# Kernel tuning notes

Hardware: AMD Instinct MI355X
Metric: run time of the kernel (lower is better)

Reference implementation:

```python
import jax, jax.numpy as jnp
import numpy as np

EPS = 1e-6  # GLOBAL_EPS
D_QK = 192
ATTN_DIM = 768


def setup_inputs() -> dict:
    key = jax.random.key(0)
    ks = jax.random.split(key, 12)
    B, C, H, W = 16, 192, 56, 56
    d_qk, d_v = D_QK, 2 * D_QK
    attn_dim, inner = ATTN_DIM, d_v
    r = lambda k, s, sc=0.05: jax.random.normal(k, s, dtype=jnp.float32) * sc
    return {
        "x": jax.random.normal(ks[0], (B, C, H, W), dtype=jnp.float32),
        "proj_w": r(ks[1], (attn_dim, C)),          # 1x1 conv + BN folded
        "proj_b": r(ks[2], (attn_dim,)),
        "dwc_w": r(ks[3], (attn_dim, 1, 3, 3)),     # depthwise 3x3, BN folded
        "dwc_b": r(ks[4], (attn_dim,)),
        "g_w": r(ks[5], (inner, attn_dim)),          # ConvGate pointwise conv1d
        "g_b": r(ks[6], (inner,)),
        "an_w": 1.0 + r(ks[7], (inner,)),            # RMSNorm weight
        "sv": 1.0 + r(ks[8], (inner,)),              # Scale(inner, (1, inner, 1))
        "out_w": r(ks[9], (C, inner)),               # 1x1 conv + BN folded
        "out_b": r(ks[10], (C,)),
    }


def reference(x, proj_w, proj_b, dwc_w, dwc_b, g_w, g_b, an_w, sv, out_w, out_b):
    B, C, H, W = x.shape
    d_qk = D_QK
    # proj: ConvNorm 1x1 (conv + BN folded to affine)
    y = jnp.einsum("bchw,oc->bohw", x, proj_w) + proj_b[None, :, None, None]
    # dwc: RepConv depthwise 3x3 with residual (res=True)
    dw = jax.lax.conv_general_dilated(
        y, dwc_w, window_strides=(1, 1), padding="SAME",
        dimension_numbers=("NCHW", "OIHW", "NCHW"),
        feature_group_count=ATTN_DIM)
    y = dw + dwc_b[None, :, None, None] + y
    # flatten spatial -> tokens, split q/k/v along channels
    xs = y.reshape(B, ATTN_DIM, H * W)            # (B, attn_dim, N)
    q, k, v = xs[:, :d_qk], xs[:, d_qk:2 * d_qk], xs[:, 2 * d_qk:]
    # linear_attn: feature map = silu, scale = N**-0.5
    qf = jax.nn.silu(q)                            # (B, d_qk, N)
    kf = jax.nn.silu(k)
    N = H * W
    s = N ** -0.5
    # use_linear branch (N >> d): z = kT.mean(-2,True) @ q + eps ; attn = (v s)(kT s) q
    z = jnp.einsum("bd,bdn->bn", kf.mean(-1), qf)[:, None, :] + EPS  # (B, 1, N)
    vk = jnp.einsum("bvn,bdn->bvd", v * s, kf * s)  # (B, d_v, d_qk)
    attn = jnp.einsum("bvd,bdn->bvn", vk, qf) / z   # (B, d_v, N)
    # gate: pointwise conv1d on full projected features + sigmoid
    gate = jax.nn.sigmoid(jnp.einsum("bcn,oc->bon", xs, g_w) + g_b[None, :, None])
    attn = attn * gate
    # attn_norm (RMS over channels) + scale_v(v) residual
    rms = jnp.sqrt(jnp.mean(attn * attn, axis=1, keepdims=True) + EPS)
    attn = attn / rms * an_w[None, :, None] + v * sv[None, :, None]
    # out: ConvNorm 1x1 back to dim
    o = attn.reshape(B, -1, H, W)
    return jnp.einsum("bchw,oc->bohw", o, out_w) + out_b[None, :, None, None]
```

## Files before the change

kernel.cpp:

```cpp
#include <hip/hip_runtime.h>
#include <hip/hip_bf16.h>

typedef unsigned short u16;
typedef __attribute__((ext_vector_type(8))) short bf16x8;
typedef __attribute__((ext_vector_type(4))) float f32x4;

constexpr int B_ = 16, C_ = 192, H_ = 56, W_ = 56;
constexpr int N_ = H_ * W_;
constexpr int A_ = 768;
constexpr int Dq = 192;
constexpr int Vd = 384;
constexpr float EPSf = 1e-6f;

union U8 { bf16x8 v; u16 s[8]; unsigned u[4]; };

__device__ __forceinline__ float bits2f(u16 u) {
  return __uint_as_float(((unsigned)u) << 16);
}
__device__ __forceinline__ u16 f2bits(float f) {
  __hip_bfloat16 h = __float2bfloat16(f);
  u16 u;
  __builtin_memcpy(&u, &h, sizeof(u));
  return u;
}
__device__ __forceinline__ float silu_f(float v) { return v / (1.0f + __expf(-v)); }
__device__ __forceinline__ float sigm_f(float v) { return 1.0f / (1.0f + __expf(-v)); }

__device__ __forceinline__ f32x4 MFMA(bf16x8 a, bf16x8 b, f32x4 c) {
  return __builtin_amdgcn_mfma_f32_16x16x32_bf16(a, b, c, 0, 0, 0);
}

__global__ __launch_bounds__(256) void k_prep(const float* __restrict__ pw,
                                              const float* __restrict__ gw,
                                              const float* __restrict__ ow,
                                              u16* __restrict__ pwb,
                                              u16* __restrict__ gwb,
                                              u16* __restrict__ owb) {
  const int bid = blockIdx.x;
  const size_t base = ((size_t)bid * 256 + threadIdx.x) * 8;
  const float* src;
  u16* dst;
  size_t off;
  if (bid < 72) { src = pw; dst = pwb; off = base; }
  else if (bid < 216) { src = gw; dst = gwb; off = base - 147456; }
  else { src = ow; dst = owb; off = base - 442368; }
  float4 v0 = *(const float4*)&src[off];
  float4 v1 = *(const float4*)&src[off + 4];
  U8 r;
  r.s[0] = f2bits(v0.x); r.s[1] = f2bits(v0.y); r.s[2] = f2bits(v0.z); r.s[3] = f2bits(v0.w);
  r.s[4] = f2bits(v1.x); r.s[5] = f2bits(v1.y); r.s[6] = f2bits(v1.z); r.s[7] = f2bits(v1.w);
  *(bf16x8*)&dst[off] = r.v;
}

__global__ __launch_bounds__(256) void k_proj(const float* __restrict__ x,
                                              const u16* __restrict__ pwb,
                                              const float* __restrict__ pb,
                                              u16* __restrict__ y0t) {
  const int n0 = blockIdx.x * 64;
  const int oy = blockIdx.y;
  const int b = blockIdx.z;
  __shared__ u16 Xt[64][200];
  __shared__ u16 Wa[256][32];
  const int t = threadIdx.x;
  const int lane = t & 63, wid = t >> 6;
  const int fr = lane & 15, fg = lane >> 4;

  {
    const int p = t & 31, co = t >> 5;
    const float* xb = x + (size_t)b * C_ * N_ + n0 + 2 * p;
#pragma unroll
    for (int rnd = 0; rnd < 3; ++rnd) {
      const int c0 = rnd * 64 + co * 8;
      float2 v[8];
#pragma unroll
      for (int i = 0; i < 8; ++i) v[i] = *(const float2*)&xb[(size_t)(c0 + i) * N_];
      U8 r0, r1;
#pragma unroll
      for (int i = 0; i < 8; ++i) { r0.s[i] = f2bits(v[i].x); r1.s[i] = f2bits(v[i].y); }
      *(bf16x8*)&Xt[2 * p][c0] = r0.v;
      *(bf16x8*)&Xt[2 * p + 1][c0] = r1.v;
    }
  }

  f32x4 acc[4][4];
#pragma unroll
  for (int mi = 0; mi < 4; ++mi)
#pragma unroll
    for (int ni = 0; ni < 4; ++ni) acc[mi][ni] = (f32x4){0.f, 0.f, 0.f, 0.f};

  const int orow_c = t >> 2, oct_c = t & 3;
  for (int ks = 0; ks < 6; ++ks) {
    __syncthreads();
#pragma unroll
    for (int jj = 0; jj < 4; ++jj) {
      const int orow = orow_c + 64 * jj;
      const int sw = (orow >> 1) & 3;
      bf16x8 v = *(const bf16x8*)&pwb[(size_t)(oy * 256 + orow) * C_ + ks * 32 + oct_c * 8];
      *(bf16x8*)&Wa[orow][(oct_c ^ sw) * 8] = v;
    }
    __syncthreads();
    bf16x8 bfrag[4];
#pragma unroll
    for (int ni = 0; ni < 4; ++ni)
      bfrag[ni] = *(const bf16x8*)&Xt[ni * 16 + fr][ks * 32 + fg * 8];
#pragma unroll
    for (int mi = 0; mi < 4; ++mi) {
      const int ar = wid * 64 + mi * 16 + fr;
      bf16x8 a = *(const bf16x8*)&Wa[ar][(fg ^ ((ar >> 1) & 3)) * 8];
#pragma unroll
      for (int ni = 0; ni < 4; ++ni) acc[mi][ni] = MFMA(a, bfrag[ni], acc[mi][ni]);
    }
  }
#pragma unroll
  for (int mi = 0; mi < 4; ++mi) {
    const int o4 = oy * 256 + wid * 64 + mi * 16 + fg * 4;
    const float b0 = pb[o4], b1 = pb[o4 + 1], b2 = pb[o4 + 2], b3 = pb[o4 + 3];
#pragma unroll
    for (int ni = 0; ni < 4; ++ni) {
      const int n = n0 + ni * 16 + fr;
      ushort4 pk;
      pk.x = f2bits(acc[mi][ni][0] + b0);
      pk.y = f2bits(acc[mi][ni][1] + b1);
      pk.z = f2bits(acc[mi][ni][2] + b2);
      pk.w = f2bits(acc[mi][ni][3] + b3);
      *(ushort4*)&y0t[((size_t)b * N_ + n) * A_ + o4] = pk;
    }
  }
}

__global__ __launch_bounds__(256) void k_dwc(const u16* __restrict__ y0t,
                                             const float* __restrict__ cw,
                                             const float* __restrict__ cb,
                                             u16* __restrict__ yt,
                                             u16* __restrict__ skq) {
  const int pid = blockIdx.x;
  const int L = (pid & 7) * 336 + (pid >> 3);
  const int h = L % 56, at = (L / 56) % 3, b = L / 168;
  const int t = threadIdx.x;
  const int a = at * 256 + (t & 31) * 8;
  const int wl = t >> 5;
  float w9[9][8];
  float bias[8];
#pragma unroll
  for (int j = 0; j < 8; ++j) {
    bias[j] = cb[a + j];
#pragma unroll
    for (int k = 0; k < 9; ++k) w9[k][j] = cw[(a + j) * 9 + k];
  }
  const u16* src = y0t + (size_t)b * N_ * A_ + a;
  u16* dst = yt + (size_t)b * N_ * A_ + a;
  const bool hok0 = h > 0, hok2 = h < 55;
  for (int wc = 0; wc < 7; ++wc) {
    const int w = wc * 8 + wl;
    const bool wok0 = w > 0, wok2 = w < 55;
    U8 nb[9];
#pragma unroll
    for (int dh = -1; dh <= 1; ++dh) {
      const bool hok = (dh == -1) ? hok0 : ((dh == 1) ? hok2 : true);
#pragma unroll
      for (int dw = -1; dw <= 1; ++dw) {
        const int k = (dh + 1) * 3 + (dw + 1);
        const bool ok = hok && ((dw == -1) ? wok0 : ((dw == 1) ? wok2 : true));
        if (ok)
          nb[k].v = *(const bf16x8*)&src[(size_t)((h + dh) * 56 + (w + dw)) * A_];
        else
          nb[k].u[0] = nb[k].u[1] = nb[k].u[2] = nb[k].u[3] = 0u;
      }
    }
    U8 o;
    float sv[8];
#pragma unroll
    for (int j = 0; j < 8; ++j) {
      float s = bias[j] + bits2f(nb[4].s[j]);
#pragma unroll
      for (int k = 0; k < 9; ++k) s = fmaf(w9[k][j], bits2f(nb[k].s[j]), s);
      sv[j] = s;
      o.s[j] = f2bits(s);
    }
    *(bf16x8*)&dst[(size_t)(h * 56 + w) * A_] = o.v;
    if (a < 384) {
      U8 q;
#pragma unroll
      for (int j = 0; j < 8; ++j) q.s[j] = f2bits(silu_f(sv[j]));
      *(bf16x8*)&skq[((size_t)b * N_ + h * 56 + w) * 384 + a] = q.v;
    }
  }
}

__global__ __launch_bounds__(256) void k_kfmean(const u16* __restrict__ skq,
                                                float* __restrict__ kfp) {
  const int ns = blockIdx.x, dc = blockIdx.y, b = blockIdx.z;
  const int t = threadIdx.x;
  const int dq = t & 15, nw = t >> 4;
  const u16* p = skq + ((size_t)b * N_ + ns * 448 + nw) * 384 + 192 + dc * 64 + dq * 4;
  float s0 = 0, s1 = 0, s2 = 0, s3 = 0;
#pragma unroll 4
  for (int i = 0; i < 28; ++i) {
    ushort4 u = *(const ushort4*)&p[(size_t)i * 16 * 384];
    s0 += bits2f(u.x);
    s1 += bits2f(u.y);
    s2 += bits2f(u.z);
    s3 += bits2f(u.w);
  }
  __shared__ float red[16][65];
  red[nw][dq * 4 + 0] = s0;
  red[nw][dq * 4 + 1] = s1;
  red[nw][dq * 4 + 2] = s2;
  red[nw][dq * 4 + 3] = s3;
  __syncthreads();
  if (t < 64) {
    float s = 0;
#pragma unroll
    for (int i = 0; i < 16; ++i) s += red[i][t];
    kfp[((size_t)ns * B_ + b) * Dq + dc * 64 + t] = s * (1.0f / (float)N_);
  }
}

__global__ __launch_bounds__(256) void k_z(const u16* __restrict__ skq,
                                           const float* __restrict__ kfp,
                                           float* __restrict__ zinv) {
  const int b = blockIdx.y;
  const int n = blockIdx.x * 256 + threadIdx.x;
  __shared__ float kf[192];
  if (threadIdx.x < 192) {
    float s = 0;
#pragma unroll
    for (int ns = 0; ns < 7; ++ns) s += kfp[((size_t)ns * B_ + b) * Dq + threadIdx.x];
    kf[threadIdx.x] = s;
  }
  __syncthreads();
  if (n < N_) {
    const u16* p = skq + ((size_t)b * N_ + n) * 384;
    float z = 0;
#pragma unroll
    for (int j = 0; j < 24; ++j) {
      U8 u;
      u.v = *(const bf16x8*)&p[j * 8];
#pragma unroll
      for (int i = 0; i < 8; ++i) z = fmaf(kf[j * 8 + i], bits2f(u.s[i]), z);
    }
    zinv[(size_t)b * N_ + n] = 1.0f / (z + EPSf);
  }
}

__global__ __launch_bounds__(256) void k_vk(const u16* __restrict__ skq,
                                            const u16* __restrict__ yt,
                                            float* __restrict__ vkpart) {
  const int pid = blockIdx.x;
  const int L = (pid & 7) * 42 + (pid >> 3);
  const int ns = L % 7;
  const int vblk = (L / 7) % 3;
  const int b = L / 21;
  const int t = threadIdx.x;
  const int lane = t & 63, wid = t >> 6;
  const int fr = lane & 15, fg = lane >> 4;
  const int vbase = (wid >> 1) * 64, dbase = (wid & 1) * 96;

  __shared__ u16 T[320 * 64];
  unsigned* T32 = (unsigned*)T;

  const int oct0 = t & 7;
  const int pair = (t >> 3) & 31;
  const int nb0 = ns * 448;

  U8 pre[5][2];
  auto load_pre = [&](int n0) {
    const int n = nb0 + n0 + pair * 2;
#pragma unroll
    for (int j = 0; j < 5; ++j) {
      const int oct = oct0 + 8 * j;
      const u16* srcp;
      size_t stride;
      if (j < 3) {
        srcp = skq + ((size_t)b * N_ + n) * 384 + 192 + oct * 8;
        stride = 384;
      } else {
        srcp = yt + ((size_t)b * N_ + n) * A_ + 384 + vblk * 128 + (oct - 24) * 8;
        stride = A_;
      }
      pre[j][0].v = *(const bf16x8*)srcp;
      pre[j][1].v = *(const bf16x8*)(srcp + stride);
    }
  };

  f32x4 acc[4][6];
#pragma unroll
  for (int mi = 0; mi < 4; ++mi)
#pragma unroll
    for (int ni = 0; ni < 6; ++ni) acc[mi][ni] = (f32x4){0.f, 0.f, 0.f, 0.f};

  load_pre(0);
  for (int s = 0; s < 7; ++s) {
    __syncthreads();
#pragma unroll
    for (int j = 0; j < 5; ++j) {
      const int rowb = (oct0 + 8 * j) * 8;
#pragma unroll
      for (int i = 0; i < 8; ++i) {
        const int row = rowb + i;
        const int sw = (row & 7) ^ ((row >> 3) & 7);
        const unsigned val =
            ((unsigned)pre[j][0].s[i] & 0xffffu) | (((unsigned)pre[j][1].s[i]) << 16);
        T32[row * 32 + (pair ^ (sw << 2))] = val;
      }
    }
    __syncthreads();
    if (s < 6) load_pre((s + 1) * 64);
#pragma unroll
    for (int kf2 = 0; kf2 < 2; ++kf2) {
      bf16x8 bfrag[6];
#pragma unroll
      for (int ni = 0; ni < 6; ++ni) {
        const int row = dbase + ni * 16 + fr;
        const int sw = (row & 7) ^ ((row >> 3) & 7);
        bfrag[ni] = *(const bf16x8*)&T[row * 64 + ((kf2 * 32 + fg * 8) ^ (sw << 3))];
      }
#pragma unroll
      for (int mi = 0; mi < 4; ++mi) {
        const int row = 192 + vbase + mi * 16 + fr;
        const int sw = (row & 7) ^ ((row >> 3) & 7);
        bf16x8 a = *(const bf16x8*)&T[row * 64 + ((kf2 * 32 + fg * 8) ^ (sw << 3))];
#pragma unroll
        for (int ni = 0; ni < 6; ++ni) acc[mi][ni] = MFMA(a, bfrag[ni], acc[mi][ni]);
      }
    }
  }
  float* base = vkpart + (((size_t)ns * 16 + b) * 3 + vblk) * (128 * 192);
#pragma unroll
  for (int mi = 0; mi < 4; ++mi)
#pragma unroll
    for (int ni = 0; ni < 6; ++ni) {
      const int v = vbase + mi * 16 + fg * 4;
      const int d = dbase + ni * 16 + fr;
      float* o = base + (size_t)v * 192 + d;
      o[0] = acc[mi][ni][0];
      o[192] = acc[mi][ni][1];
      o[384] = acc[mi][ni][2];
      o[576] = acc[mi][ni][3];
    }
}

__global__ __launch_bounds__(256) void k_vkred(const float* __restrict__ vkpart,
                                               u16* __restrict__ vkb) {
  const size_t e = ((size_t)blockIdx.x * 256 + threadIdx.x) * 8;
  constexpr size_t NSSTRIDE = (size_t)16 * 3 * 128 * 192;
  float4 s0 = {0, 0, 0, 0}, s1 = {0, 0, 0, 0};
#pragma unroll
  for (int ns = 0; ns < 7; ++ns) {
    float4 a0 = *(const float4*)&vkpart[ns * NSSTRIDE + e];
    float4 a1 = *(const float4*)&vkpart[ns * NSSTRIDE + e + 4];
    s0.x += a0.x; s0.y += a0.y; s0.z += a0.z; s0.w += a0.w;
    s1.x += a1.x; s1.y += a1.y; s1.z += a1.z; s1.w += a1.w;
  }
  const float sc = 1.0f / (float)N_;
  U8 r;
  r.s[0] = f2bits(s0.x * sc); r.s[1] = f2bits(s0.y * sc);
  r.s[2] = f2bits(s0.z * sc); r.s[3] = f2bits(s0.w * sc);
  r.s[4] = f2bits(s1.x * sc); r.s[5] = f2bits(s1.y * sc);
  r.s[6] = f2bits(s1.z * sc); r.s[7] = f2bits(s1.w * sc);
  *(bf16x8*)&vkb[e] = r.v;
}

__global__ __launch_bounds__(256, 3) void k_gateattn(const u16* __restrict__ yt,
                                                     const u16* __restrict__ skq,
                                                     const float* __restrict__ zinv,
                                                     const u16* __restrict__ vkb,
                                                     const u16* __restrict__ gwb,
                                                     const float* __restrict__ gb,
                                                     u16* __restrict__ attnt) {
  const int pid = blockIdx.x;
  const int L = (pid & 7) * 196 + (pid >> 3);
  const int vh = L & 1;
  const int n0 = ((L >> 1) % 49) * 64;
  const int b = L / 98;
  const int t = threadIdx.x;
  const int lane = t & 63, wid = t >> 6, wm = wid >> 1, wn = wid & 1;
  const int fr = lane & 15, fg = lane >> 4;
  __shared__ u16 Wa[192][40];
  __shared__ u16 Xt[64][40];
  __shared__ float zl[64];
  if (t < 64) zl[t] = zinv[(size_t)b * N_ + n0 + t];
  const u16* yb = yt + ((size_t)b * N_ + n0) * A_;
  const u16* qb = skq + ((size_t)b * N_ + n0) * 384;

  f32x4 acc[6][2];
#pragma unroll
  for (int mi = 0; mi < 6; ++mi)
#pragma unroll
    for (int ni = 0; ni < 2; ++ni) acc[mi][ni] = (f32x4){0.f, 0.f, 0.f, 0.f};

  for (int ks = 0; ks < 6; ++ks) {
    {
      const int o = t >> 2, cs = t & 3;
#pragma unroll
      for (int rr = 0; rr < 3; ++rr) {
        const int v = rr * 64 + o;
        *(bf16x8*)&Wa[v][cs * 8] =
            *(const bf16x8*)&vkb[((size_t)(vh * 192 + v) + 0) * 0 +
                                 ((size_t)b * Vd + vh * 192 + v) * 192 + ks * 32 + cs * 8];
      }
    }
    {
      const int n = t >> 2, aq = t & 3;
      *(bf16x8*)&Xt[n][aq * 8] = *(const bf16x8*)&qb[(size_t)n * 384 + ks * 32 + aq * 8];
    }
    __syncthreads();
    bf16x8 bfr[2];
#pragma unroll
    for (int ni = 0; ni < 2; ++ni) bfr[ni] = *(const bf16x8*)&Xt[wn * 32 + ni * 16 + fr][fg * 8];
#pragma unroll
    for (int mi = 0; mi < 6; ++mi) {
      bf16x8 a = *(const bf16x8*)&Wa[wm * 96 + mi * 16 + fr][fg * 8];
      acc[mi][0] = MFMA(a, bfr[0], acc[mi][0]);
      acc[mi][1] = MFMA(a, bfr[1], acc[mi][1]);
    }
    __syncthreads();
  }

  uint2 pp[6][2];
#pragma unroll
  for (int mi = 0; mi < 6; ++mi)
#pragma unroll
    for (int ni = 0; ni < 2; ++ni) {
      const float z = zl[wn * 32 + ni * 16 + fr];
      unsigned a0 = ((unsigned)f2bits(acc[mi][ni][0] * z) & 0xffffu) |
                    (((unsigned)f2bits(acc[mi][ni][1] * z) & 0xffffu) << 16);
      unsigned a1 = ((unsigned)f2bits(acc[mi][ni][2] * z) & 0xffffu) |
                    (((unsigned)f2bits(acc[mi][ni][3] * z) & 0xffffu) << 16);
      pp[mi][ni] = make_uint2(a0, a1);
      acc[mi][ni] = (f32x4){0.f, 0.f, 0.f, 0.f};
    }

  for (int ks = 0; ks < 24; ++ks) {
    {
      const int o = t >> 2, cs = t & 3;
#pragma unroll
      for (int rr = 0; rr < 3; ++rr) {
        const int v = rr * 64 + o;
        *(bf16x8*)&Wa[v][cs * 8] =
            *(const bf16x8*)&gwb[(size_t)(vh * 192 + v) * A_ + ks * 32 + cs * 8];
      }
    }
    {
      const int n = t >> 2, aq = t & 3;
      *(bf16x8*)&Xt[n][aq * 8] = *(const bf16x8*)&yb[(size_t)n * A_ + ks * 32 + aq * 8];
    }
    __syncthreads();
    bf16x8 bfr[2];
#pragma unroll
    for (int ni = 0; ni < 2; ++ni) bfr[ni] = *(const bf16x8*)&Xt[wn * 32 + ni * 16 + fr][fg * 8];
#pragma unroll
    for (int mi = 0; mi < 6; ++mi) {
      bf16x8 a = *(const bf16x8*)&Wa[wm * 96 + mi * 16 + fr][fg * 8];
      acc[mi][0] = MFMA(a, bfr[0], acc[mi][0]);
      acc[mi][1] = MFMA(a, bfr[1], acc[mi][1]);
    }
    __syncthreads();
  }

#pragma unroll
  for (int mi = 0; mi < 6; ++mi) {
    const int vb = vh * 192 + wm * 96 + mi * 16 + fg * 4;
    const float g0 = gb[vb], g1 = gb[vb + 1], g2 = gb[vb + 2], g3 = gb[vb + 3];
#pragma unroll
    for (int ni = 0; ni < 2; ++ni) {
      const int n = n0 + wn * 32 + ni * 16 + fr;
      const uint2 p = pp[mi][ni];
      const float pv0 = bits2f((u16)(p.x & 0xffffu)), pv1 = bits2f((u16)(p.x >> 16));
      const float pv2 = bits2f((u16)(p.y & 0xffffu)), pv3 = bits2f((u16)(p.y >> 16));
      ushort4 o;
      o.x = f2bits(pv0 * sigm_f(acc[mi][ni][0] + g0));
      o.y = f2bits(pv1 * sigm_f(acc[mi][ni][1] + g1));
      o.z = f2bits(pv2 * sigm_f(acc[mi][ni][2] + g2));
      o.w = f2bits(pv3 * sigm_f(acc[mi][ni][3] + g3));
      *(ushort4*)&attnt[((size_t)b * N_ + n) * Vd + vb] = o;
    }
  }
}

__global__ __launch_bounds__(256) void k_rmsfinal(const u16* __restrict__ yt,
                                                  const float* __restrict__ anw,
                                                  const float* __restrict__ svw,
                                                  u16* __restrict__ attnt) {
  const int b = blockIdx.y;
  const int n0 = blockIdx.x * 32;
  const int t = threadIdx.x;
  __shared__ float anws[384], svws[384];
  for (int i = t; i < 384; i += 256) {
    anws[i] = anw[i];
    svws[i] = svw[i];
  }
  __syncthreads();
  const int n = n0 + (t >> 3);
  const int vs = (t & 7) * 8;
  u16* ap = attnt + ((size_t)b * N_ + n) * Vd;
  U8 av[6];
  float ss = 0.f;
#pragma unroll
  for (int j = 0; j < 6; ++j) {
    av[j].v = *(const bf16x8*)&ap[vs + j * 64];
#pragma unroll
    for (int i = 0; i < 8; ++i) {
      const float f = bits2f(av[j].s[i]);
      ss = fmaf(f, f, ss);
    }
  }
  ss += __shfl_xor(ss, 1);
  ss += __shfl_xor(ss, 2);
  ss += __shfl_xor(ss, 4);
  const float rinv = rsqrtf(ss * (1.0f / (float)Vd) + EPSf);
  const u16* vp = yt + ((size_t)b * N_ + n) * A_ + 2 * Dq;
#pragma unroll
  for (int j = 0; j < 6; ++j) {
    U8 vv, o;
    vv.v = *(const bf16x8*)&vp[vs + j * 64];
#pragma unroll
    for (int i = 0; i < 8; ++i) {
      const int v = vs + j * 64 + i;
      const float val = bits2f(av[j].s[i]) * rinv * anws[v] + bits2f(vv.s[i]) * svws[v];
      o.s[i] = f2bits(val);
    }
    *(bf16x8*)&ap[vs + j * 64] = o.v;
  }
}

__global__ __launch_bounds__(256, 2) void k_out(const u16* __restrict__ attnt,
                                                const u16* __restrict__ owb,
                                                const float* __restrict__ ob,
                                                float* __restrict__ out) {
  const int n0 = blockIdx.x * 64;
  const int b = blockIdx.y;
  __shared__ u16 Xt[64][392];
  __shared__ u16 Wa[64][40];
  const int t = threadIdx.x;
  const int lane = t & 63, wid = t >> 6, wm = wid >> 1, wn = wid & 1;
  const int fr = lane & 15, fg = lane >> 4;
  {
    const int n = t >> 2, aq = t & 3;
    const u16* src = attnt + ((size_t)b * N_ + n0 + n) * Vd + aq * 8;
#pragma unroll
    for (int vr = 0; vr < 12; ++vr)
      *(bf16x8*)&Xt[n][vr * 32 + aq * 8] = *(const bf16x8*)&src[vr * 32];
  }
  f32x4 acc[2][2];
  for (int cb = 0; cb < 3; ++cb) {
#pragma unroll
    for (int mi = 0; mi < 2; ++mi)
#pragma unroll
      for (int ni = 0; ni < 2; ++ni) acc[mi][ni] = (f32x4){0.f, 0.f, 0.f, 0.f};
    for (int ks = 0; ks < 12; ++ks) {
      {
        const int o = t >> 2, cs = t & 3;
        *(bf16x8*)&Wa[o][cs * 8] =
            *(const bf16x8*)&owb[(size_t)(cb * 64 + o) * Vd + ks * 32 + cs * 8];
      }
      __syncthreads();
      bf16x8 a0 = *(const bf16x8*)&Wa[wm * 32 + fr][fg * 8];
      bf16x8 a1 = *(const bf16x8*)&Wa[wm * 32 + 16 + fr][fg * 8];
      bf16x8 b0 = *(const bf16x8*)&Xt[wn * 32 + fr][ks * 32 + fg * 8];
      bf16x8 b1 = *(const bf16x8*)&Xt[wn * 32 + 16 + fr][ks * 32 + fg * 8];
      acc[0][0] = MFMA(a0, b0, acc[0][0]);
      acc[0][1] = MFMA(a0, b1, acc[0][1]);
      acc[1][0] = MFMA(a1, b0, acc[1][0]);
      acc[1][1] = MFMA(a1, b1, acc[1][1]);
      __syncthreads();
    }
#pragma unroll
    for (int mi = 0; mi < 2; ++mi) {
      const int c = cb * 64 + wm * 32 + mi * 16 + fg * 4;
      const float b0 = ob[c], b1 = ob[c + 1], b2 = ob[c + 2], b3 = ob[c + 3];
#pragma unroll
      for (int ni = 0; ni < 2; ++ni) {
        const int n = n0 + wn * 32 + ni * 16 + fr;
        float* o = out + ((size_t)b * C_ + c) * N_ + n;
        o[0 * N_] = acc[mi][ni][0] + b0;
        o[1 * N_] = acc[mi][ni][1] + b1;
        o[2 * N_] = acc[mi][ni][2] + b2;
        o[3 * N_] = acc[mi][ni][3] + b3;
      }
    }
  }
}

extern "C" void kernel_launch(void* const* d_in, const int* in_sizes, int n_in,
                              void* d_out, int out_size, void* d_ws, size_t ws_size,
                              hipStream_t stream) {
  (void)in_sizes; (void)n_in; (void)out_size; (void)ws_size;
  const float* x = (const float*)d_in[0];
  const float* pw = (const float*)d_in[1];
  const float* pb = (const float*)d_in[2];
  const float* cw = (const float*)d_in[3];
  const float* cb = (const float*)d_in[4];
  const float* gw = (const float*)d_in[5];
  const float* gb = (const float*)d_in[6];
  const float* anw = (const float*)d_in[7];
  const float* svw = (const float*)d_in[8];
  const float* ow = (const float*)d_in[9];
  const float* ob = (const float*)d_in[10];
  float* out = (float*)d_out;

  char* ws = (char*)d_ws;
  const size_t szY = (size_t)B_ * N_ * A_ * 2;
  u16* y0t = (u16*)(ws);
  u16* attnt = (u16*)(ws);
  float* vkpart = (float*)(ws + 38535168);
  u16* vkb = (u16*)(ws + 71565312);
  u16* yt = (u16*)(ws + szY);
  u16* skq = (u16*)(ws + 2 * szY);
  char* ws2 = ws + 2 * szY + 38535168;
  float* kfp = (float*)(ws2);
  float* zinv = (float*)(ws2 + 86016);
  u16* pwb = (u16*)(ws2 + 86016 + 200704);
  u16* gwb = (u16*)(ws2 + 86016 + 200704 + 294912);
  u16* owb = (u16*)(ws2 + 86016 + 200704 + 294912 + 589824);

  k_prep<<<dim3(252), 256, 0, stream>>>(pw, gw, ow, pwb, gwb, owb);
  k_proj<<<dim3(49, 3, 16), 256, 0, stream>>>(x, pwb, pb, y0t);
  k_dwc<<<dim3(2688), 256, 0, stream>>>(y0t, cw, cb, yt, skq);
  k_kfmean<<<dim3(7, 3, 16), 256, 0, stream>>>(skq, kfp);
  k_z<<<dim3(13, 16), 256, 0, stream>>>(skq, kfp, zinv);
  k_vk<<<dim3(336), 256, 0, stream>>>(skq, yt, vkpart);
  k_vkred<<<dim3(576), 256, 0, stream>>>(vkpart, vkb);
  k_gateattn<<<dim3(1568), 256, 0, stream>>>(yt, skq, zinv, vkb, gwb, gb, attnt);
  k_rmsfinal<<<dim3(98, 16), 256, 0, stream>>>(yt, anw, svw, attnt);
  k_out<<<dim3(49, 16), 256, 0, stream>>>(attnt, owb, ob, out);
}
```

Measured before the change: 316.1 us.

## Register-prefetch global tiles and widen K steps in GEMM kernels

Measured after the change: 272.6 us. 1.16x faster.

```diff
diff --git a/kernel.cpp b/kernel.cpp
--- a/kernel.cpp
+++ b/kernel.cpp
@@ -89,20 +89,31 @@
     for (int ni = 0; ni < 4; ++ni) acc[mi][ni] = (f32x4){0.f, 0.f, 0.f, 0.f};
 
   const int orow_c = t >> 2, oct_c = t & 3;
+  U8 wreg[4];
+#pragma unroll
+  for (int jj = 0; jj < 4; ++jj)
+    wreg[jj].v = *(const bf16x8*)&pwb[(size_t)(oy * 256 + orow_c + 64 * jj) * C_ + oct_c * 8];
+
   for (int ks = 0; ks < 6; ++ks) {
     __syncthreads();
 #pragma unroll
     for (int jj = 0; jj < 4; ++jj) {
       const int orow = orow_c + 64 * jj;
       const int sw = (orow >> 1) & 3;
-      bf16x8 v = *(const bf16x8*)&pwb[(size_t)(oy * 256 + orow) * C_ + ks * 32 + oct_c * 8];
-      *(bf16x8*)&Wa[orow][(oct_c ^ sw) * 8] = v;
-    }
-    __syncthreads();
+      *(bf16x8*)&Wa[orow][(oct_c ^ sw) * 8] = wreg[jj].v;
+    }
+    __syncthreads();
+    if (ks < 5) {
+#pragma unroll
+      for (int jj = 0; jj < 4; ++jj)
+        wreg[jj].v = *(const bf16x8*)&pwb[(size_t)(oy * 256 + orow_c + 64 * jj) * C_ +
+                                          (ks + 1) * 32 + oct_c * 8];
+    }
     bf16x8 bfrag[4];
 #pragma unroll
     for (int ni = 0; ni < 4; ++ni)
       bfrag[ni] = *(const bf16x8*)&Xt[ni * 16 + fr][ks * 32 + fg * 8];
+    __builtin_amdgcn_s_setprio(1);
 #pragma unroll
     for (int mi = 0; mi < 4; ++mi) {
       const int ar = wid * 64 + mi * 16 + fr;
@@ -110,6 +121,7 @@
 #pragma unroll
       for (int ni = 0; ni < 4; ++ni) acc[mi][ni] = MFMA(a, bfrag[ni], acc[mi][ni]);
     }
+    __builtin_amdgcn_s_setprio(0);
   }
 #pragma unroll
   for (int mi = 0; mi < 4; ++mi) {
@@ -306,6 +318,7 @@
     }
     __syncthreads();
     if (s < 6) load_pre((s + 1) * 64);
+    __builtin_amdgcn_s_setprio(1);
 #pragma unroll
     for (int kf2 = 0; kf2 < 2; ++kf2) {
       bf16x8 bfrag[6];
@@ -324,6 +337,7 @@
         for (int ni = 0; ni < 6; ++ni) acc[mi][ni] = MFMA(a, bfrag[ni], acc[mi][ni]);
       }
     }
+    __builtin_amdgcn_s_setprio(0);
   }
   float* base = vkpart + (((size_t)ns * 16 + b) * 3 + vblk) * (128 * 192);
 #pragma unroll
@@ -361,13 +375,13 @@
   *(bf16x8*)&vkb[e] = r.v;
 }
 
-__global__ __launch_bounds__(256, 3) void k_gateattn(const u16* __restrict__ yt,
-                                                     const u16* __restrict__ skq,
-                                                     const float* __restrict__ zinv,
-                                                     const u16* __restrict__ vkb,
-                                                     const u16* __restrict__ gwb,
-                                                     const float* __restrict__ gb,
-                                                     u16* __restrict__ attnt) {
+__global__ __launch_bounds__(256) void k_gateattn(const u16* __restrict__ yt,
+                                                  const u16* __restrict__ skq,
+                                                  const float* __restrict__ zinv,
+                                                  const u16* __restrict__ vkb,
+                                                  const u16* __restrict__ gwb,
+                                                  const float* __restrict__ gb,
+                                                  u16* __restrict__ attnt) {
   const int pid = blockIdx.x;
   const int L = (pid & 7) * 196 + (pid >> 3);
   const int vh = L & 1;
@@ -376,86 +390,92 @@
   const int t = threadIdx.x;
   const int lane = t & 63, wid = t >> 6, wm = wid >> 1, wn = wid & 1;
   const int fr = lane & 15, fg = lane >> 4;
-  __shared__ u16 Wa[192][40];
-  __shared__ u16 Xt[64][40];
+  __shared__ u16 Wa[192][104];
+  __shared__ u16 Xt[64][104];
   __shared__ float zl[64];
   if (t < 64) zl[t] = zinv[(size_t)b * N_ + n0 + t];
   const u16* yb = yt + ((size_t)b * N_ + n0) * A_;
   const u16* qb = skq + ((size_t)b * N_ + n0) * 384;
+  const u16* wb0 = vkb + ((size_t)b * Vd + vh * 192) * 192;
+  const u16* wb1 = gwb + (size_t)(vh * 192) * A_;
+
+  int wrow[9], woc[9];
+#pragma unroll
+  for (int j = 0; j < 9; ++j) { const int idx = j * 256 + t; wrow[j] = idx / 12; woc[j] = idx % 12; }
+  int xrow[3], xoc[3];
+#pragma unroll
+  for (int j = 0; j < 3; ++j) { const int idx = j * 256 + t; xrow[j] = idx / 12; xoc[j] = idx % 12; }
+
+  U8 wreg[9], xreg[3];
+  auto loadW = [&](int ph, int ks0) {
+#pragma unroll
+    for (int j = 0; j < 9; ++j) {
+      const u16* s = ph ? (wb1 + (size_t)wrow[j] * A_ + ks0 + woc[j] * 8)
+                        : (wb0 + (size_t)wrow[j] * 192 + ks0 + woc[j] * 8);
+      wreg[j].v = *(const bf16x8*)s;
+    }
+  };
+  auto loadX = [&](int ph, int ks0) {
+#pragma unroll
+    for (int j = 0; j < 3; ++j) {
+      const u16* s = ph ? (yb + (size_t)xrow[j] * A_ + ks0 + xoc[j] * 8)
+                        : (qb + (size_t)xrow[j] * 384 + ks0 + xoc[j] * 8);
+      xreg[j].v = *(const bf16x8*)s;
+    }
+  };
 
   f32x4 acc[6][2];
 #pragma unroll
   for (int mi = 0; mi < 6; ++mi)
 #pragma unroll
     for (int ni = 0; ni < 2; ++ni) acc[mi][ni] = (f32x4){0.f, 0.f, 0.f, 0.f};
-
-  for (int ks = 0; ks < 6; ++ks) {
-    {
-      const int o = t >> 2, cs = t & 3;
-#pragma unroll
-      for (int rr = 0; rr < 3; ++rr) {
-        const int v = rr * 64 + o;
-        *(bf16x8*)&Wa[v][cs * 8] =
-            *(const bf16x8*)&vkb[((size_t)(vh * 192 + v) + 0) * 0 +
-                                 ((size_t)b * Vd + vh * 192 + v) * 192 + ks * 32 + cs * 8];
+  uint2 pp[6][2];
+
+  loadW(0, 0);
+  loadX(0, 0);
+  for (int it = 0; it < 10; ++it) {
+    __syncthreads();
+#pragma unroll
+    for (int j = 0; j < 9; ++j) *(bf16x8*)&Wa[wrow[j]][woc[j] * 8] = wreg[j].v;
+#pragma unroll
+    for (int j = 0; j < 3; ++j) *(bf16x8*)&Xt[xrow[j]][xoc[j] * 8] = xreg[j].v;
+    __syncthreads();
+    if (it < 9) {
+      const int nit = it + 1;
+      const int ph = nit >= 2;
+      const int ks0 = ph ? (nit - 2) * 96 : nit * 96;
+      loadW(ph, ks0);
+      loadX(ph, ks0);
+    }
+    __builtin_amdgcn_s_setprio(1);
+#pragma unroll
+    for (int kf = 0; kf < 3; ++kf) {
+      bf16x8 bfr[2];
+#pragma unroll
+      for (int ni = 0; ni < 2; ++ni)
+        bfr[ni] = *(const bf16x8*)&Xt[wn * 32 + ni * 16 + fr][kf * 32 + fg * 8];
+#pragma unroll
+      for (int mi = 0; mi < 6; ++mi) {
+        bf16x8 a = *(const bf16x8*)&Wa[wm * 96 + mi * 16 + fr][kf * 32 + fg * 8];
+        acc[mi][0] = MFMA(a, bfr[0], acc[mi][0]);
+        acc[mi][1] = MFMA(a, bfr[1], acc[mi][1]);
       }
     }
-    {
-      const int n = t >> 2, aq = t & 3;
-      *(bf16x8*)&Xt[n][aq * 8] = *(const bf16x8*)&qb[(size_t)n * 384 + ks * 32 + aq * 8];
-    }
-    __syncthreads();
-    bf16x8 bfr[2];
-#pragma unroll
-    for (int ni = 0; ni < 2; ++ni) bfr[ni] = *(const bf16x8*)&Xt[wn * 32 + ni * 16 + fr][fg * 8];
-#pragma unroll
-    for (int mi = 0; mi < 6; ++mi) {
-      bf16x8 a = *(const bf16x8*)&Wa[wm * 96 + mi * 16 + fr][fg * 8];
-      acc[mi][0] = MFMA(a, bfr[0], acc[mi][0]);
-      acc[mi][1] = MFMA(a, bfr[1], acc[mi][1]);
-    }
-    __syncthreads();
-  }
-
-  uint2 pp[6][2];
-#pragma unroll
-  for (int mi = 0; mi < 6; ++mi)
-#pragma unroll
-    for (int ni = 0; ni < 2; ++ni) {
-      const float z = zl[wn * 32 + ni * 16 + fr];
-      unsigned a0 = ((unsigned)f2bits(acc[mi][ni][0] * z) & 0xffffu) |
-                    (((unsigned)f2bits(acc[mi][ni][1] * z) & 0xffffu) << 16);
-      unsigned a1 = ((unsigned)f2bits(acc[mi][ni][2] * z) & 0xffffu) |
-                    (((unsigned)f2bits(acc[mi][ni][3] * z) & 0xffffu) << 16);
-      pp[mi][ni] = make_uint2(a0, a1);
-      acc[mi][ni] = (f32x4){0.f, 0.f, 0.f, 0.f};
-    }
-
-  for (int ks = 0; ks < 24; ++ks) {
-    {
-      const int o = t >> 2, cs = t & 3;
-#pragma unroll
-      for (int rr = 0; rr < 3; ++rr) {
-        const int v = rr * 64 + o;
-        *(bf16x8*)&Wa[v][cs * 8] =
-            *(const bf16x8*)&gwb[(size_t)(vh * 192 + v) * A_ + ks * 32 + cs * 8];
-      }
-    }
-    {
-      const int n = t >> 2, aq = t & 3;
-      *(bf16x8*)&Xt[n][aq * 8] = *(const bf16x8*)&yb[(size_t)n * A_ + ks * 32 + aq * 8];
-    }
-    __syncthreads();
-    bf16x8 bfr[2];
-#pragma unroll
-    for (int ni = 0; ni < 2; ++ni) bfr[ni] = *(const bf16x8*)&Xt[wn * 32 + ni * 16 + fr][fg * 8];
-#pragma unroll
-    for (int mi = 0; mi < 6; ++mi) {
-      bf16x8 a = *(const bf16x8*)&Wa[wm * 96 + mi * 16 + fr][fg * 8];
-      acc[mi][0] = MFMA(a, bfr[0], acc[mi][0]);
-      acc[mi][1] = MFMA(a, bfr[1], acc[mi][1]);
-    }
-    __syncthreads();
+    __builtin_amdgcn_s_setprio(0);
+    if (it == 1) {
+#pragma unroll
+      for (int mi = 0; mi < 6; ++mi)
+#pragma unroll
+        for (int ni = 0; ni < 2; ++ni) {
+          const float z = zl[wn * 32 + ni * 16 + fr];
+          unsigned a0 = ((unsigned)f2bits(acc[mi][ni][0] * z) & 0xffffu) |
+                        (((unsigned)f2bits(acc[mi][ni][1] * z) & 0xffffu) << 16);
+          unsigned a1 = ((unsigned)f2bits(acc[mi][ni][2] * z) & 0xffffu) |
+                        (((unsigned)f2bits(acc[mi][ni][3] * z) & 0xffffu) << 16);
+          pp[mi][ni] = make_uint2(a0, a1);
+          acc[mi][ni] = (f32x4){0.f, 0.f, 0.f, 0.f};
+        }
+    }
   }
 
 #pragma unroll
@@ -524,60 +544,85 @@
   }
 }
 
-__global__ __launch_bounds__(256, 2) void k_out(const u16* __restrict__ attnt,
-                                                const u16* __restrict__ owb,
-                                                const float* __restrict__ ob,
-                                                float* __restrict__ out) {
+__global__ __launch_bounds__(256) void k_out(const u16* __restrict__ attnt,
+                                             const u16* __restrict__ owb,
+                                             const float* __restrict__ ob,
+                                             float* __restrict__ out) {
   const int n0 = blockIdx.x * 64;
   const int b = blockIdx.y;
-  __shared__ u16 Xt[64][392];
-  __shared__ u16 Wa[64][40];
+  __shared__ u16 Wa[192][104];
+  __shared__ u16 Xt[64][104];
   const int t = threadIdx.x;
   const int lane = t & 63, wid = t >> 6, wm = wid >> 1, wn = wid & 1;
   const int fr = lane & 15, fg = lane >> 4;
-  {
-    const int n = t >> 2, aq = t & 3;
-    const u16* src = attnt + ((size_t)b * N_ + n0 + n) * Vd + aq * 8;
-#pragma unroll
-    for (int vr = 0; vr < 12; ++vr)
-      *(bf16x8*)&Xt[n][vr * 32 + aq * 8] = *(const bf16x8*)&src[vr * 32];
-  }
-  f32x4 acc[2][2];
-  for (int cb = 0; cb < 3; ++cb) {
-#pragma unroll
-    for (int mi = 0; mi < 2; ++mi)
-#pragma unroll
-      for (int ni = 0; ni < 2; ++ni) acc[mi][ni] = (f32x4){0.f, 0.f, 0.f, 0.f};
-    for (int ks = 0; ks < 12; ++ks) {
-      {
-        const int o = t >> 2, cs = t & 3;
-        *(bf16x8*)&Wa[o][cs * 8] =
-            *(const bf16x8*)&owb[(size_t)(cb * 64 + o) * Vd + ks * 32 + cs * 8];
+  const u16* xb = attnt + ((size_t)b * N_ + n0) * Vd;
+
+  int wrow[9], woc[9];
+#pragma unroll
+  for (int j = 0; j < 9; ++j) { const int idx = j * 256 + t; wrow[j] = idx / 12; woc[j] = idx % 12; }
+  int xrow[3], xoc[3];
+#pragma unroll
+  for (int j = 0; j < 3; ++j) { const int idx = j * 256 + t; xrow[j] = idx / 12; xoc[j] = idx % 12; }
+
+  U8 wreg[9], xreg[3];
+  auto loadW = [&](int ks0) {
+#pragma unroll
+    for (int j = 0; j < 9; ++j)
+      wreg[j].v = *(const bf16x8*)&owb[(size_t)wrow[j] * Vd + ks0 + woc[j] * 8];
+  };
+  auto loadX = [&](int ks0) {
+#pragma unroll
+    for (int j = 0; j < 3; ++j)
+      xreg[j].v = *(const bf16x8*)&xb[(size_t)xrow[j] * Vd + ks0 + xoc[j] * 8];
+  };
+
+  f32x4 acc[6][2];
+#pragma unroll
+  for (int mi = 0; mi < 6; ++mi)
+#pragma unroll
+    for (int ni = 0; ni < 2; ++ni) acc[mi][ni] = (f32x4){0.f, 0.f, 0.f, 0.f};
+
+  loadW(0);
+  loadX(0);
+  for (int it = 0; it < 4; ++it) {
+    __syncthreads();
+#pragma unroll
+    for (int j = 0; j < 9; ++j) *(bf16x8*)&Wa[wrow[j]][woc[j] * 8] = wreg[j].v;
+#pragma unroll
+    for (int j = 0; j < 3; ++j) *(bf16x8*)&Xt[xrow[j]][xoc[j] * 8] = xreg[j].v;
+    __syncthreads();
+    if (it < 3) {
+      loadW((it + 1) * 96);
+      loadX((it + 1) * 96);
+    }
+    __builtin_amdgcn_s_setprio(1);
+#pragma unroll
+    for (int kf = 0; kf < 3; ++kf) {
+      bf16x8 bfr[2];
+#pragma unroll
+      for (int ni = 0; ni < 2; ++ni)
+        bfr[ni] = *(const bf16x8*)&Xt[wn * 32 + ni * 16 + fr][kf * 32 + fg * 8];
+#pragma unroll
+      for (int mi = 0; mi < 6; ++mi) {
+        bf16x8 a = *(const bf16x8*)&Wa[wm * 96 + mi * 16 + fr][kf * 32 + fg * 8];
+        acc[mi][0] = MFMA(a, bfr[0], acc[mi][0]);
+        acc[mi][1] = MFMA(a, bfr[1], acc[mi][1]);
       }
-      __syncthreads();
-      bf16x8 a0 = *(const bf16x8*)&Wa[wm * 32 + fr][fg * 8];
-      bf16x8 a1 = *(const bf16x8*)&Wa[wm * 32 + 16 + fr][fg * 8];
-      bf16x8 b0 = *(const bf16x8*)&Xt[wn * 32 + fr][ks * 32 + fg * 8];
-      bf16x8 b1 = *(const bf16x8*)&Xt[wn * 32 + 16 + fr][ks * 32 + fg * 8];
-      acc[0][0] = MFMA(a0, b0, acc[0][0]);
-      acc[0][1] = MFMA(a0, b1, acc[0][1]);
-      acc[1][0] = MFMA(a1, b0, acc[1][0]);
-      acc[1][1] = MFMA(a1, b1, acc[1][1]);
-      __syncthreads();
-    }
-#pragma unroll
-    for (int mi = 0; mi < 2; ++mi) {
-      const int c = cb * 64 + wm * 32 + mi * 16 + fg * 4;
-      const float b0 = ob[c], b1 = ob[c + 1], b2 = ob[c + 2], b3 = ob[c + 3];
-#pragma unroll
-      for (int ni = 0; ni < 2; ++ni) {
-        const int n = n0 + wn * 32 + ni * 16 + fr;
-        float* o = out + ((size_t)b * C_ + c) * N_ + n;
-        o[0 * N_] = acc[mi][ni][0] + b0;
-        o[1 * N_] = acc[mi][ni][1] + b1;
-        o[2 * N_] = acc[mi][ni][2] + b2;
-        o[3 * N_] = acc[mi][ni][3] + b3;
-      }
+    }
+    __builtin_amdgcn_s_setprio(0);
+  }
+#pragma unroll
+  for (int mi = 0; mi < 6; ++mi) {
+    const int c = wm * 96 + mi * 16 + fg * 4;
+    const float b0 = ob[c], b1 = ob[c + 1], b2 = ob[c + 2], b3 = ob[c + 3];
+#pragma unroll
+    for (int ni = 0; ni < 2; ++ni) {
+      const int n = n0 + wn * 32 + ni * 16 + fr;
+      float* o = out + ((size_t)b * C_ + c) * N_ + n;
+      o[0 * N_] = acc[mi][ni][0] + b0;
+      o[1 * N_] = acc[mi][ni][1] + b1;
+      o[2 * N_] = acc[mi][ni][2] + b2;
+      o[3 * N_] = acc[mi][ni][3] + b3;
     }
   }
 }
```
